# Kernel optimization log

Measured on AMD Instinct MI355X. Metric: run time of the kernel, lower is better.

The kernel has to match this reference:

```python
import jax, jax.numpy as jnp
import numpy as np

T, B, D, H = 256, 128, 128, 1024
MEL = 48           # preprocess.melodyRange
MELODY_COEFF = 0.5
FORGET_BIAS = 1.0  # TF BasicLSTMCell default


def setup_inputs() -> dict:
    key = jax.random.key(0)
    ks = jax.random.split(key, 8)
    s = 0.05
    return {
        "inSeq": jax.random.normal(ks[0], (T, B, D), dtype=jnp.float32),
        "targetSeq": jax.random.randint(ks[1], (T, B, 2), 0, MEL).astype(jnp.int64),
        "W1": jax.random.normal(ks[2], (D + H, 4 * H), dtype=jnp.float32) * s,
        "b1": jnp.zeros((4 * H,), dtype=jnp.float32),
        "W2": jax.random.normal(ks[3], (2 * H, 4 * H), dtype=jnp.float32) * s,
        "b2": jnp.zeros((4 * H,), dtype=jnp.float32),
        "outW": jax.random.normal(ks[4], (H, D), dtype=jnp.float32) * s,
        "outB": jnp.zeros((D,), dtype=jnp.float32),
    }


def _lstm_cell(x, c, h, W, b):
    # TF BasicLSTMCell: gates in (i, j, f, o) order, forget_bias added to f
    z = jnp.concatenate([x, h], axis=-1) @ W + b
    i, j, f, o = jnp.split(z, 4, axis=-1)
    c_new = c * jax.nn.sigmoid(f + FORGET_BIAS) + jax.nn.sigmoid(i) * jnp.tanh(j)
    h_new = jnp.tanh(c_new) * jax.nn.sigmoid(o)
    return c_new, h_new


def _forward(inSeq, targetSeq, W1, b1, W2, b2, outW, outB):
    dt = inSeq.dtype
    zero = jnp.zeros((B, H), dtype=dt)

    def step(carry, x):
        c1, h1, c2, h2 = carry
        c1, h1 = _lstm_cell(x, c1, h1, W1, b1)
        c2, h2 = _lstm_cell(h1, c2, h2, W2, b2)
        return (c1, h1, c2, h2), h2

    _, outputs = jax.lax.scan(step, (zero, zero, zero, zero), inSeq)  # [T,B,H]
    logits = outputs @ outW + outB                                    # [T,B,D]

    mel_logits = logits[..., :MEL]
    har_logits = logits[..., MEL:]

    # probs: per-timestep dual softmax, concatenated
    probs = jnp.concatenate(
        [jax.nn.softmax(mel_logits, axis=-1), jax.nn.softmax(har_logits, axis=-1)],
        axis=-1,
    )

    # dual sparse softmax cross-entropy
    mel_lp = jax.nn.log_softmax(mel_logits, axis=-1)
    har_lp = jax.nn.log_softmax(har_logits, axis=-1)
    mel_ce = -jnp.take_along_axis(mel_lp, targetSeq[..., 0:1], axis=-1)[..., 0]
    har_ce = -jnp.take_along_axis(har_lp, targetSeq[..., 1:2], axis=-1)[..., 0]
    losses = MELODY_COEFF * mel_ce + (1.0 - MELODY_COEFF) * har_ce
    loss = jnp.sum(losses) / T / B
    return probs, loss


def reference(inSeq, targetSeq, W1, b1, W2, b2, outW, outB):
    return _forward(inSeq, targetSeq, W1, b1, W2, b2, outW, outB)
```

## Files before the change

kernel.cpp:

```cpp
#include <hip/hip_runtime.h>
#include <cstdint>
#include <cstddef>

#define T_ 256
#define B_ 128
#define D_ 128
#define H_ 1024
#define K1_ 1152
#define K2_ 2048

typedef __bf16 bf16x8 __attribute__((ext_vector_type(8)));
typedef short s8 __attribute__((ext_vector_type(8)));
typedef float f32x4 __attribute__((ext_vector_type(4)));

__device__ __forceinline__ unsigned short f2bf(float f) {
  unsigned int u = __builtin_bit_cast(unsigned int, f);
  u += 0x7fff + ((u >> 16) & 1);
  return (unsigned short)(u >> 16);
}
__device__ __forceinline__ float sigm(float x) { return 1.f / (1.f + __expf(-x)); }
__device__ __forceinline__ float tanh_(float x) { return 1.f - 2.f / (__expf(2.f * x) + 1.f); }

__device__ __forceinline__ f32x4 mfma16(s8 a, s8 b, f32x4 c) {
  return __builtin_amdgcn_mfma_f32_16x16x32_bf16(
      __builtin_bit_cast(bf16x8, a), __builtin_bit_cast(bf16x8, b), c, 0, 0, 0);
}

__global__ void prep_misc(const float* __restrict__ inSeq,
                          const float* __restrict__ outW,
                          unsigned short* __restrict__ xbf,
                          unsigned short* __restrict__ outWp,
                          unsigned short* __restrict__ h1b,
                          unsigned short* __restrict__ h2all,
                          float* __restrict__ c1, float* __restrict__ c2,
                          float* __restrict__ loss)
{
  int i = blockIdx.x * 256 + threadIdx.x;
  if (i < T_ * B_ * D_) xbf[i] = f2bf(inSeq[i]);
  if (i < B_ * H_) {
    c1[i] = 0.f; c2[i] = 0.f;
    h1b[B_ * H_ + i] = 0;
    h2all[i] = 0;
  }
  if (i < H_ * D_) {
    int c = i >> 10, k = i & 1023;
    outWp[i] = f2bf(outW[(size_t)k * D_ + c]);
  }
  if (i == 0) loss[0] = 0.f;
}

__global__ void pack_w(const float* __restrict__ src, unsigned short* __restrict__ dst, int K)
{
  __shared__ float tile[64][65];
  int k0 = blockIdx.x * 64, j0 = blockIdx.y * 64, g = blockIdx.z;
  int tid = threadIdx.x;
#pragma unroll
  for (int e = 0; e < 16; ++e) {
    int li = e * 256 + tid;
    int kl = li >> 6, jl = li & 63;
    tile[kl][jl] = src[(size_t)(k0 + kl) * 4096 + g * 1024 + j0 + jl];
  }
  __syncthreads();
#pragma unroll
  for (int e = 0; e < 16; ++e) {
    int li = e * 256 + tid;
    int jl = li >> 6, kl = li & 63;
    dst[(size_t)((j0 + jl) * 4 + g) * K + k0 + kl] = f2bf(tile[kl][jl]);
  }
}

__global__ __launch_bounds__(256, 2) void phase_kernel(
    int p,
    const unsigned short* __restrict__ xbf,
    const unsigned short* __restrict__ W1p,
    const unsigned short* __restrict__ W2p,
    const float* __restrict__ b1,
    const float* __restrict__ b2,
    unsigned short* __restrict__ h1b,
    unsigned short* __restrict__ h2all,
    float* __restrict__ c1,
    float* __restrict__ c2)
{
  __shared__ float red[4][2048];
  const int bid = blockIdx.x;
  const bool isL2 = bid >= 256;
  if (!isL2 && p >= T_) return;
  if (isL2 && p == 0) return;
  const int jb = isL2 ? (bid - 256) : bid;
  const int mt = jb & 1, nt = jb >> 1;
  const int t = isL2 ? (p - 1) : p;
  const int r0 = mt * 64, c0 = nt * 32;
  const int tid = threadIdx.x;
  const int wid = tid >> 6, lane = tid & 63;
  const int quad = lane >> 4, l15 = lane & 15;
  const int kseg = quad * 8;

  const unsigned short* hsrc = h1b + (size_t)((p + 1) & 1) * (B_ * H_);

  f32x4 acc[4][2];
#pragma unroll
  for (int i = 0; i < 4; ++i)
#pragma unroll
    for (int j = 0; j < 2; ++j) acc[i][j] = (f32x4){0.f, 0.f, 0.f, 0.f};

  int arow[4], bcol[2];
#pragma unroll
  for (int i = 0; i < 4; ++i) arow[i] = r0 + i * 16 + l15;
#pragma unroll
  for (int j = 0; j < 2; ++j) bcol[j] = c0 + j * 16 + l15;

  if (!isL2) {
    const unsigned short* xt = xbf + (size_t)t * (B_ * D_);
    const int cpw = 9;
    const int kcbase = wid * cpw;
    s8 a[4], b[2], an[4], bn[2];
    auto LD = [&](int kc, s8* A, s8* Bv) {
      int kk = kc * 32 + kseg;
      if (kk < D_) {
#pragma unroll
        for (int i = 0; i < 4; ++i) A[i] = *(const s8*)(xt + (size_t)arow[i] * D_ + kk);
      } else {
#pragma unroll
        for (int i = 0; i < 4; ++i) A[i] = *(const s8*)(hsrc + (size_t)arow[i] * H_ + (kk - D_));
      }
#pragma unroll
      for (int j = 0; j < 2; ++j) Bv[j] = *(const s8*)(W1p + (size_t)bcol[j] * K1_ + kk);
    };
    LD(kcbase, a, b);
    for (int c = 0; c < cpw; ++c) {
      if (c + 1 < cpw) LD(kcbase + c + 1, an, bn);
#pragma unroll
      for (int i = 0; i < 4; ++i)
#pragma unroll
        for (int j = 0; j < 2; ++j) acc[i][j] = mfma16(a[i], b[j], acc[i][j]);
#pragma unroll
      for (int i = 0; i < 4; ++i) a[i] = an[i];
      b[0] = bn[0]; b[1] = bn[1];
    }
  } else {
    const unsigned short* h2prev = h2all + (size_t)t * (B_ * H_);
    const int cpw = 16;
    const int kcbase = wid * cpw;
    s8 a[4], b[2], an[4], bn[2];
    auto LD = [&](int kc, s8* A, s8* Bv) {
      int kk = kc * 32 + kseg;
      if (kk < H_) {
#pragma unroll
        for (int i = 0; i < 4; ++i) A[i] = *(const s8*)(hsrc + (size_t)arow[i] * H_ + kk);
      } else {
#pragma unroll
        for (int i = 0; i < 4; ++i) A[i] = *(const s8*)(h2prev + (size_t)arow[i] * H_ + (kk - H_));
      }
#pragma unroll
      for (int j = 0; j < 2; ++j) Bv[j] = *(const s8*)(W2p + (size_t)bcol[j] * K2_ + kk);
    };
    LD(kcbase, a, b);
    for (int c = 0; c < cpw; ++c) {
      if (c + 1 < cpw) LD(kcbase + c + 1, an, bn);
#pragma unroll
      for (int i = 0; i < 4; ++i)
#pragma unroll
        for (int j = 0; j < 2; ++j) acc[i][j] = mfma16(a[i], b[j], acc[i][j]);
#pragma unroll
      for (int i = 0; i < 4; ++i) a[i] = an[i];
      b[0] = bn[0]; b[1] = bn[1];
    }
  }

#pragma unroll
  for (int i = 0; i < 4; ++i)
#pragma unroll
    for (int j = 0; j < 2; ++j)
#pragma unroll
      for (int r = 0; r < 4; ++r)
        red[wid][(i * 16 + quad * 4 + r) * 32 + (j * 16 + l15)] = acc[i][j][r];
  __syncthreads();
#pragma unroll
  for (int it = 0; it < 8; ++it) {
    int e = it * 256 + tid;
    red[0][e] = red[0][e] + red[1][e] + red[2][e] + red[3][e];
  }
  __syncthreads();

  const float* bias = isL2 ? b2 : b1;
  float* cst = isL2 ? c2 : c1;
  unsigned short* hout = isL2 ? (h2all + (size_t)(t + 1) * (B_ * H_))
                              : (h1b + (size_t)(p & 1) * (B_ * H_));
#pragma unroll
  for (int it = 0; it < 2; ++it) {
    int s = it * 256 + tid;
    int row = s >> 3, u = s & 7;
    int jg = (c0 >> 2) + u;
    float zi = red[0][row * 32 + u * 4 + 0] + bias[0 * H_ + jg];
    float zj = red[0][row * 32 + u * 4 + 1] + bias[1 * H_ + jg];
    float zf = red[0][row * 32 + u * 4 + 2] + bias[2 * H_ + jg];
    float zo = red[0][row * 32 + u * 4 + 3] + bias[3 * H_ + jg];
    int rg = r0 + row;
    float co = cst[(size_t)rg * H_ + jg];
    float cn = co * sigm(zf + 1.0f) + sigm(zi) * tanh_(zj);
    float hn = tanh_(cn) * sigm(zo);
    cst[(size_t)rg * H_ + jg] = cn;
    hout[(size_t)rg * H_ + jg] = f2bf(hn);
  }
}

__global__ __launch_bounds__(256, 1) void proj_kernel(
    const unsigned short* __restrict__ h2flat,
    const unsigned short* __restrict__ outWp,
    const float* __restrict__ outB,
    const int* __restrict__ targets,
    float* __restrict__ out,
    float* __restrict__ loss)
{
  __shared__ float lg[128][129];
  __shared__ float red2[256];
  const int r0 = blockIdx.x * 128;
  const int tid = threadIdx.x;
  const int wid = tid >> 6, lane = tid & 63;
  const int quad = lane >> 4, l15 = lane & 15;
  const int wr = (wid & 1) * 64, wc = (wid >> 1) * 64;
  const int kseg = quad * 8;

  f32x4 acc[4][4];
#pragma unroll
  for (int i = 0; i < 4; ++i)
#pragma unroll
    for (int j = 0; j < 4; ++j) acc[i][j] = (f32x4){0.f, 0.f, 0.f, 0.f};

  int arow[4], bcolv[4];
#pragma unroll
  for (int i = 0; i < 4; ++i) arow[i] = r0 + wr + i * 16 + l15;
#pragma unroll
  for (int j = 0; j < 4; ++j) bcolv[j] = wc + j * 16 + l15;

  s8 a[4], b[4], an[4], bn[4];
  auto LD = [&](int kc, s8* A, s8* Bv) {
    int kk = kc * 32 + kseg;
#pragma unroll
    for (int i = 0; i < 4; ++i) A[i] = *(const s8*)(h2flat + (size_t)arow[i] * H_ + kk);
#pragma unroll
    for (int j = 0; j < 4; ++j) Bv[j] = *(const s8*)(outWp + (size_t)bcolv[j] * H_ + kk);
  };
  LD(0, a, b);
  for (int c = 0; c < 32; ++c) {
    if (c + 1 < 32) LD(c + 1, an, bn);
#pragma unroll
    for (int i = 0; i < 4; ++i)
#pragma unroll
      for (int j = 0; j < 4; ++j) acc[i][j] = mfma16(a[i], b[j], acc[i][j]);
#pragma unroll
    for (int i = 0; i < 4; ++i) a[i] = an[i];
#pragma unroll
    for (int j = 0; j < 4; ++j) b[j] = bn[j];
  }

#pragma unroll
  for (int i = 0; i < 4; ++i)
#pragma unroll
    for (int j = 0; j < 4; ++j)
#pragma unroll
      for (int r = 0; r < 4; ++r)
        lg[wr + i * 16 + quad * 4 + r][wc + j * 16 + l15] = acc[i][j][r] + outB[bcolv[j]];
  __syncthreads();

  const int row = tid >> 1, half = tid & 1;
  const int cbeg = half ? 48 : 0, cend = half ? 128 : 48;
  float m = -1e30f;
  for (int c = cbeg; c < cend; ++c) m = fmaxf(m, lg[row][c]);
  float s = 0.f;
  for (int c = cbeg; c < cend; ++c) s += __expf(lg[row][c] - m);
  float rinv = 1.f / s;
  float* orow = out + (size_t)(r0 + row) * D_;
  for (int c = cbeg; c < cend; ++c) orow[c] = __expf(lg[row][c] - m) * rinv;

  int tg = targets[(size_t)(r0 + row) * 2 + half];
  int tc = half ? (48 + tg) : tg;
  float ce = -(lg[row][tc] - m - logf(s));
  red2[tid] = 0.5f * ce;
  __syncthreads();
  for (int o = 128; o > 0; o >>= 1) {
    if (tid < o) red2[tid] += red2[tid + o];
    __syncthreads();
  }
  if (tid == 0) atomicAdd(loss, red2[0]);
}

__global__ void finalize_loss(const float* __restrict__ loss, float* __restrict__ out)
{
  out[(size_t)T_ * B_ * D_] = loss[0] * (1.f / (float)(T_ * B_));
}

extern "C" void kernel_launch(void* const* d_in, const int* in_sizes, int n_in,
                              void* d_out, int out_size, void* d_ws, size_t ws_size,
                              hipStream_t stream)
{
  const float* inSeq = (const float*)d_in[0];
  const int* targets = (const int*)d_in[1];
  const float* W1 = (const float*)d_in[2];
  const float* b1 = (const float*)d_in[3];
  const float* W2 = (const float*)d_in[4];
  const float* b2 = (const float*)d_in[5];
  const float* outW = (const float*)d_in[6];
  const float* outB = (const float*)d_in[7];
  float* out = (float*)d_out;

  char* w = (char*)d_ws;
  auto alloc = [&](size_t bytes) {
    char* r = w;
    w += (bytes + 255) & ~(size_t)255;
    return r;
  };
  unsigned short* W1p = (unsigned short*)alloc((size_t)4096 * K1_ * 2);
  unsigned short* W2p = (unsigned short*)alloc((size_t)4096 * K2_ * 2);
  unsigned short* xbf = (unsigned short*)alloc((size_t)T_ * B_ * D_ * 2);
  unsigned short* h1b = (unsigned short*)alloc((size_t)2 * B_ * H_ * 2);
  unsigned short* h2all = (unsigned short*)alloc((size_t)(T_ + 1) * B_ * H_ * 2);
  float* c1 = (float*)alloc((size_t)B_ * H_ * 4);
  float* c2 = (float*)alloc((size_t)B_ * H_ * 4);
  unsigned short* outWp = (unsigned short*)alloc((size_t)H_ * D_ * 2);
  float* loss = (float*)alloc(256);

  prep_misc<<<dim3((T_ * B_ * D_) / 256), dim3(256), 0, stream>>>(
      inSeq, outW, xbf, outWp, h1b, h2all, c1, c2, loss);
  pack_w<<<dim3(K1_ / 64, 16, 4), dim3(256), 0, stream>>>(W1, W1p, K1_);
  pack_w<<<dim3(K2_ / 64, 16, 4), dim3(256), 0, stream>>>(W2, W2p, K2_);

  for (int p = 0; p <= T_; ++p)
    phase_kernel<<<dim3(512), dim3(256), 0, stream>>>(
        p, xbf, W1p, W2p, b1, b2, h1b, h2all, c1, c2);

  proj_kernel<<<dim3(256), dim3(256), 0, stream>>>(
      h2all + (size_t)B_ * H_, outWp, outB, targets, out, loss);
  finalize_loss<<<dim3(1), dim3(1), 0, stream>>>(loss, out);
}
```

Baseline: 5.756 ms.

## Replace per-timestep kernel launches with persistent cooperative LSTM kernel

```diff
diff --git a/kernel.cpp b/kernel.cpp
--- a/kernel.cpp
+++ b/kernel.cpp
@@ -1,6 +1,9 @@
 #include <hip/hip_runtime.h>
+#include <hip/hip_cooperative_groups.h>
 #include <cstdint>
 #include <cstddef>
+
+namespace cg = cooperative_groups;
 
 #define T_ 256
 #define B_ 128
@@ -201,6 +204,190 @@
     float hn = tanh_(cn) * sigm(zo);
     cst[(size_t)rg * H_ + jg] = cn;
     hout[(size_t)rg * H_ + jg] = f2bf(hn);
+  }
+}
+
+__global__ __launch_bounds__(256, 2) void lstm_persistent(
+    const unsigned short* __restrict__ xbf,
+    const unsigned short* __restrict__ W1p,
+    const unsigned short* __restrict__ W2p,
+    const float* __restrict__ b1,
+    const float* __restrict__ b2,
+    unsigned short* __restrict__ h1b,
+    unsigned short* __restrict__ h2all)
+{
+  cg::grid_group gg = cg::this_grid();
+  __shared__ float red[4][2048];
+  const int bid = blockIdx.x;
+  const bool isL2 = bid >= 256;
+  const int jb = isL2 ? (bid - 256) : bid;
+  const int mt = jb & 1, nt = jb >> 1;
+  const int r0 = mt * 64, c0 = nt * 32;
+  const int tid = threadIdx.x;
+  const int wid = tid >> 6, lane = tid & 63;
+  const int quad = lane >> 4, l15 = lane & 15;
+  const int kseg = quad * 8;
+
+  int arow[4], bcol[2];
+#pragma unroll
+  for (int i = 0; i < 4; ++i) arow[i] = r0 + i * 16 + l15;
+#pragma unroll
+  for (int j = 0; j < 2; ++j) bcol[j] = c0 + j * 16 + l15;
+
+  const float* bias = isL2 ? b2 : b1;
+  int ridx[2];
+  unsigned hoff[2];
+  float bz[2][4], creg[2];
+#pragma unroll
+  for (int it = 0; it < 2; ++it) {
+    int s = it * 256 + tid;
+    int row = s >> 3, u = s & 7;
+    int jg = (c0 >> 2) + u;
+    ridx[it] = row * 32 + u * 4;
+    hoff[it] = (unsigned)((r0 + row) * H_ + jg);
+#pragma unroll
+    for (int g = 0; g < 4; ++g) bz[it][g] = bias[g * H_ + jg];
+    creg[it] = 0.f;
+  }
+
+  if (!isL2) {
+    const int kcbase = wid * 9;
+    s8 bw[9][2];
+#pragma unroll
+    for (int c = 0; c < 9; ++c) {
+      int kk = (kcbase + c) * 32 + kseg;
+      bw[c][0] = *(const s8*)(W1p + (size_t)bcol[0] * K1_ + kk);
+      bw[c][1] = *(const s8*)(W1p + (size_t)bcol[1] * K1_ + kk);
+    }
+    for (int p = 0; p <= T_; ++p) {
+      if (p < T_) {
+        const unsigned short* hsrc = h1b + (size_t)((p + 1) & 1) * (B_ * H_);
+        const unsigned short* xt = xbf + (size_t)p * (B_ * D_);
+        f32x4 acc[4][2];
+#pragma unroll
+        for (int i = 0; i < 4; ++i)
+#pragma unroll
+          for (int j = 0; j < 2; ++j) acc[i][j] = (f32x4){0.f, 0.f, 0.f, 0.f};
+        s8 a[4], an[4];
+        auto LD = [&](int kc, s8* A) {
+          int kk = kc * 32 + kseg;
+          if (kk < D_) {
+#pragma unroll
+            for (int i = 0; i < 4; ++i) A[i] = *(const s8*)(xt + (size_t)arow[i] * D_ + kk);
+          } else {
+#pragma unroll
+            for (int i = 0; i < 4; ++i) A[i] = *(const s8*)(hsrc + (size_t)arow[i] * H_ + (kk - D_));
+          }
+        };
+        LD(kcbase, a);
+#pragma unroll
+        for (int c = 0; c < 9; ++c) {
+          if (c + 1 < 9) LD(kcbase + c + 1, an);
+#pragma unroll
+          for (int i = 0; i < 4; ++i)
+#pragma unroll
+            for (int j = 0; j < 2; ++j) acc[i][j] = mfma16(a[i], bw[c][j], acc[i][j]);
+#pragma unroll
+          for (int i = 0; i < 4; ++i) a[i] = an[i];
+        }
+#pragma unroll
+        for (int i = 0; i < 4; ++i)
+#pragma unroll
+          for (int j = 0; j < 2; ++j)
+#pragma unroll
+            for (int r = 0; r < 4; ++r)
+              red[wid][(i * 16 + quad * 4 + r) * 32 + (j * 16 + l15)] = acc[i][j][r];
+        __syncthreads();
+#pragma unroll
+        for (int it = 0; it < 8; ++it) {
+          int e = it * 256 + tid;
+          red[0][e] = red[0][e] + red[1][e] + red[2][e] + red[3][e];
+        }
+        __syncthreads();
+        unsigned short* hout = h1b + (size_t)(p & 1) * (B_ * H_);
+#pragma unroll
+        for (int it = 0; it < 2; ++it) {
+          float zi = red[0][ridx[it] + 0] + bz[it][0];
+          float zj = red[0][ridx[it] + 1] + bz[it][1];
+          float zf = red[0][ridx[it] + 2] + bz[it][2];
+          float zo = red[0][ridx[it] + 3] + bz[it][3];
+          float cn = creg[it] * sigm(zf + 1.0f) + sigm(zi) * tanh_(zj);
+          float hn = tanh_(cn) * sigm(zo);
+          creg[it] = cn;
+          hout[hoff[it]] = f2bf(hn);
+        }
+      }
+      if (p < T_) gg.sync();
+    }
+  } else {
+    const int kcbase = wid * 16;
+    s8 bw[16][2];
+#pragma unroll
+    for (int c = 0; c < 16; ++c) {
+      int kk = (kcbase + c) * 32 + kseg;
+      bw[c][0] = *(const s8*)(W2p + (size_t)bcol[0] * K2_ + kk);
+      bw[c][1] = *(const s8*)(W2p + (size_t)bcol[1] * K2_ + kk);
+    }
+    for (int p = 0; p <= T_; ++p) {
+      if (p >= 1) {
+        const unsigned short* hsrc = h1b + (size_t)((p + 1) & 1) * (B_ * H_);
+        const unsigned short* h2prev = h2all + (size_t)(p - 1) * (B_ * H_);
+        f32x4 acc[4][2];
+#pragma unroll
+        for (int i = 0; i < 4; ++i)
+#pragma unroll
+          for (int j = 0; j < 2; ++j) acc[i][j] = (f32x4){0.f, 0.f, 0.f, 0.f};
+        s8 a[4], an[4];
+        auto LD = [&](int kc, s8* A) {
+          int kk = kc * 32 + kseg;
+          if (kk < H_) {
+#pragma unroll
+            for (int i = 0; i < 4; ++i) A[i] = *(const s8*)(hsrc + (size_t)arow[i] * H_ + kk);
+          } else {
+#pragma unroll
+            for (int i = 0; i < 4; ++i) A[i] = *(const s8*)(h2prev + (size_t)arow[i] * H_ + (kk - H_));
+          }
+        };
+        LD(kcbase, a);
+#pragma unroll
+        for (int c = 0; c < 16; ++c) {
+          if (c + 1 < 16) LD(kcbase + c + 1, an);
+#pragma unroll
+          for (int i = 0; i < 4; ++i)
+#pragma unroll
+            for (int j = 0; j < 2; ++j) acc[i][j] = mfma16(a[i], bw[c][j], acc[i][j]);
+#pragma unroll
+          for (int i = 0; i < 4; ++i) a[i] = an[i];
+        }
+#pragma unroll
+        for (int i = 0; i < 4; ++i)
+#pragma unroll
+          for (int j = 0; j < 2; ++j)
+#pragma unroll
+            for (int r = 0; r < 4; ++r)
+              red[wid][(i * 16 + quad * 4 + r) * 32 + (j * 16 + l15)] = acc[i][j][r];
+        __syncthreads();
+#pragma unroll
+        for (int it = 0; it < 8; ++it) {
+          int e = it * 256 + tid;
+          red[0][e] = red[0][e] + red[1][e] + red[2][e] + red[3][e];
+        }
+        __syncthreads();
+        unsigned short* hout = h2all + (size_t)p * (B_ * H_);
+#pragma unroll
+        for (int it = 0; it < 2; ++it) {
+          float zi = red[0][ridx[it] + 0] + bz[it][0];
+          float zj = red[0][ridx[it] + 1] + bz[it][1];
+          float zf = red[0][ridx[it] + 2] + bz[it][2];
+          float zo = red[0][ridx[it] + 3] + bz[it][3];
+          float cn = creg[it] * sigm(zf + 1.0f) + sigm(zi) * tanh_(zj);
+          float hn = tanh_(cn) * sigm(zo);
+          creg[it] = cn;
+          hout[hoff[it]] = f2bf(hn);
+        }
+      }
+      if (p < T_) gg.sync();
+    }
   }
 }
 
@@ -325,9 +512,16 @@
   pack_w<<<dim3(K1_ / 64, 16, 4), dim3(256), 0, stream>>>(W1, W1p, K1_);
   pack_w<<<dim3(K2_ / 64, 16, 4), dim3(256), 0, stream>>>(W2, W2p, K2_);
 
-  for (int p = 0; p <= T_; ++p)
-    phase_kernel<<<dim3(512), dim3(256), 0, stream>>>(
-        p, xbf, W1p, W2p, b1, b2, h1b, h2all, c1, c2);
+  void* kargs[] = {(void*)&xbf, (void*)&W1p, (void*)&W2p, (void*)&b1,
+                   (void*)&b2,  (void*)&h1b, (void*)&h2all};
+  hipError_t ce = hipLaunchCooperativeKernel((const void*)lstm_persistent,
+                                             dim3(512), dim3(256), kargs, 0, stream);
+  if (ce != hipSuccess) {
+    (void)hipGetLastError();
+    for (int p = 0; p <= T_; ++p)
+      phase_kernel<<<dim3(512), dim3(256), 0, stream>>>(
+          p, xbf, W1p, W2p, b1, b2, h1b, h2all, c1, c2);
+  }
 
   proj_kernel<<<dim3(256), dim3(256), 0, stream>>>(
       h2all + (size_t)B_ * H_, outWp, outB, targets, out, loss);
```

Result: slower. 18.32 ms (+218.2%).
